# Kernel tuning notes

Measured on AMD Instinct MI355X. Metric: run time of the kernel, lower is better.

Reference implementation:

```python
import jax, jax.numpy as jnp
import numpy as np

B, NN, HL = 64, 64, 50
IN_DIM, POS_DIM, ATT_DIM = 384, 64, 256
NEWS_DIM = IN_DIM + POS_DIM  # 448


def setup_inputs() -> dict:
    key = jax.random.key(0)
    ks = jax.random.split(key, 8)
    pos_emb = jax.random.uniform(ks[3], (100, POS_DIM), jnp.float32, -0.1, 0.1)
    pos_emb = pos_emb.at[0].set(0.0)  # initialize() zeros row 0
    return {
        "log_vec": jax.random.normal(ks[0], (B, HL, IN_DIM), jnp.float32),
        "log_mask": jax.random.randint(ks[1], (B, HL), 0, 2, jnp.int32),
        "news_vec": jax.random.normal(ks[2], (B, NN, IN_DIM), jnp.float32),
        "pos_emb": pos_emb,
        "W1": jax.random.normal(ks[4], (ATT_DIM, 2 * NEWS_DIM), jnp.float32) * 0.02,
        "b1": jnp.zeros((ATT_DIM,), jnp.float32),
        "W2": jax.random.normal(ks[5], (1, ATT_DIM), jnp.float32) * 0.02,
        "b2": jnp.zeros((1,), jnp.float32),
    }


def reference(log_vec, log_mask, news_vec, pos_emb, W1, b1, W2, b2):
    b, nn_ = news_vec.shape[:2]
    hl = log_mask.shape[1]
    # append position embeddings (row 0 for candidates, rows 1..hl for history)
    nf = jnp.concatenate(
        [news_vec, jnp.broadcast_to(pos_emb[0], (b, nn_, POS_DIM))], axis=-1)   # (B,NN,ND)
    lf = jnp.concatenate(
        [log_vec, jnp.broadcast_to(pos_emb[1:hl + 1], (b, hl, POS_DIM))], axis=-1)  # (B,HL,ND)
    # affine1(cat[news, log]) == news @ Wn^T + log @ Wl^T + b1 (avoids concat)
    Wn, Wl = W1[:, :NEWS_DIM], W1[:, NEWS_DIM:]
    pn = jnp.einsum('bnd,ad->bna', nf, Wn)   # (B,NN,A)
    pl = jnp.einsum('bhd,ad->bha', lf, Wl)   # (B,HL,A)
    h = jnp.tanh(pn[:, :, None, :] + pl[:, None, :, :] + b1)  # (B,NN,HL,A)
    logits = jnp.einsum('bnha,a->bnh', h, W2[0]) + b2[0]      # (B,NN,HL)
    logits = jnp.where(log_mask[:, None, :] == 0, jnp.float32(-1e9), logits)
    attn = jax.nn.softmax(logits, axis=2)
    user_log_vecs = jnp.einsum('bnh,bhd->bnd', attn, lf)      # (B,NN,ND)
    return user_log_vecs, nf
```

## Files before the change

### kernel.cpp

```cpp
#include <hip/hip_runtime.h>
#include <math.h>

typedef unsigned short u16;
typedef unsigned int   u32;

#define B_       64
#define NN_      64
#define HL_      50
#define IN_DIM   384
#define POS_DIM  64
#define ATT_DIM  256
#define NEWS_DIM 448

typedef __attribute__((ext_vector_type(8))) short short8;
typedef __attribute__((ext_vector_type(4))) float f32x4;

#if __has_builtin(__builtin_amdgcn_exp2f)
#define EXP2F(x) __builtin_amdgcn_exp2f(x)
#else
#define EXP2F(x) exp2f(x)
#endif
#if __has_builtin(__builtin_amdgcn_rcpf)
#define RCPF(x) __builtin_amdgcn_rcpf(x)
#else
#define RCPF(x) (1.0f/(x))
#endif

__device__ __forceinline__ u16 f2bf(float f) {
    union { float f; u32 i; } v; v.f = f;
    u32 r = v.i + 0x7fffu + ((v.i >> 16) & 1u);
    return (u16)(r >> 16);
}
__device__ __forceinline__ uint2 pack4(float4 v) {
    return make_uint2((u32)f2bf(v.x) | ((u32)f2bf(v.y) << 16),
                      (u32)f2bf(v.z) | ((u32)f2bf(v.w) << 16));
}
__device__ __forceinline__ float fast_tanh(float x) {
    float e = EXP2F(x * 2.88539008f);
    return 1.0f - 2.0f * RCPF(1.0f + e);
}

#define C_W   57344u
#define C_NV  393216u
#define C_LG  307200u
#define C_PS  51200u
#define C_NZ  65536u
#define C_LTZ 28672u
#define C_TOT (C_W + C_NV + C_LG + C_PS + C_NZ + C_LTZ)

__global__ __launch_bounds__(256) void prep_k(
    const float* __restrict__ W1, const float* __restrict__ newsv,
    const float* __restrict__ logv, const float* __restrict__ pos,
    u16* __restrict__ Wbf, u16* __restrict__ nv_bf, u16* __restrict__ lf_bf,
    u16* __restrict__ lfT_bf, float* __restrict__ nf)
{
    u32 i = blockIdx.x * 256u + threadIdx.x;
    if (i < C_W) {
        float4 v = *(const float4*)(W1 + (size_t)i * 4u);
        *(uint2*)(Wbf + (size_t)i * 4u) = pack4(v);
        return;
    }
    i -= C_W;
    if (i < C_NV) {
        float4 v = *(const float4*)(newsv + (size_t)i * 4u);
        *(uint2*)(nv_bf + (size_t)i * 4u) = pack4(v);
        u32 e = i * 4u, r = e / IN_DIM, d = e - r * IN_DIM;
        *(float4*)(nf + (size_t)r * NEWS_DIM + d) = v;
        return;
    }
    i -= C_NV;
    if (i < C_LG) {
        float4 v = *(const float4*)(logv + (size_t)i * 4u);
        u32 e = i * 4u, r = e / IN_DIM, d = e - r * IN_DIM;
        *(uint2*)(lf_bf + (size_t)r * NEWS_DIM + d) = pack4(v);
        u32 b = r / HL_, h = r - b * HL_;
        u16* t = lfT_bf + ((size_t)b * NEWS_DIM + d) * 64u + h;
        t[0]   = f2bf(v.x); t[64]  = f2bf(v.y);
        t[128] = f2bf(v.z); t[192] = f2bf(v.w);
        return;
    }
    i -= C_LG;
    if (i < C_PS) {
        u32 e = i * 4u, r = e / POS_DIM, d = e - r * POS_DIM;
        u32 b = r / HL_, h = r - b * HL_;
        float4 v = *(const float4*)(pos + (size_t)(1u + h) * POS_DIM + d);
        *(uint2*)(lf_bf + (size_t)r * NEWS_DIM + IN_DIM + d) = pack4(v);
        u16* t = lfT_bf + ((size_t)b * NEWS_DIM + IN_DIM + d) * 64u + h;
        t[0]   = f2bf(v.x); t[64]  = f2bf(v.y);
        t[128] = f2bf(v.z); t[192] = f2bf(v.w);
        return;
    }
    i -= C_PS;
    if (i < C_NZ) {
        u32 e = i * 4u, r = e / POS_DIM, d = e - r * POS_DIM;
        *(float4*)(nf + (size_t)r * NEWS_DIM + IN_DIM + d) = make_float4(0.f, 0.f, 0.f, 0.f);
        return;
    }
    i -= C_NZ;
    if (i < C_LTZ) {
        u32* t = (u32*)lfT_bf + (size_t)i * 32u + 25u;
#pragma unroll
        for (int j = 0; j < 7; j++) t[j] = 0u;
    }
}

__global__ __launch_bounds__(64) void gemm_k(
    const u16* __restrict__ nv_bf, const u16* __restrict__ lf_bf,
    const u16* __restrict__ Wbf, const float* __restrict__ b1,
    float* __restrict__ pn, float* __restrict__ plT)
{
    int bid = blockIdx.x;
    int lane = threadIdx.x;
    int m = lane & 15, q = lane >> 4;
    bool is_pn = bid < 256;
    int r0, c0, lda, koff, klen;
    const u16* A;
    if (is_pn) { r0 = (bid & 63) * 64;       c0 = (bid >> 6) * 64; A = nv_bf; lda = IN_DIM;   koff = 0;        klen = IN_DIM; }
    else { int b2 = bid - 256; r0 = (b2 % 50) * 64; c0 = (b2 / 50) * 64; A = lf_bf; lda = NEWS_DIM; koff = NEWS_DIM; klen = NEWS_DIM; }

    f32x4 acc[4][4];
#pragma unroll
    for (int a = 0; a < 4; a++)
#pragma unroll
        for (int b = 0; b < 4; b++) acc[a][b] = (f32x4){0.f, 0.f, 0.f, 0.f};

    const u16* Ap = A + (size_t)(r0 + m) * lda + q * 8;
    const u16* Wp = Wbf + (size_t)(c0 + m) * (2 * NEWS_DIM) + koff + q * 8;

    for (int k = 0; k < klen; k += 32) {
        short8 af[4], wf[4];
#pragma unroll
        for (int rt = 0; rt < 4; rt++) af[rt] = *(const short8*)(Ap + rt * 16 * lda + k);
#pragma unroll
        for (int ct = 0; ct < 4; ct++) wf[ct] = *(const short8*)(Wp + ct * 16 * (2 * NEWS_DIM) + k);
#pragma unroll
        for (int rt = 0; rt < 4; rt++)
#pragma unroll
            for (int ct = 0; ct < 4; ct++)
                acc[rt][ct] = __builtin_amdgcn_mfma_f32_16x16x32_bf16(
                    af[rt], wf[ct], acc[rt][ct], 0, 0, 0);
    }
#pragma unroll
    for (int rt = 0; rt < 4; rt++)
#pragma unroll
        for (int ct = 0; ct < 4; ct++)
#pragma unroll
            for (int i = 0; i < 4; i++) {
                int gr = r0 + rt * 16 + q * 4 + i;
                int gc = c0 + ct * 16 + m;
                float v = acc[rt][ct][i];
                if (is_pn) {
                    pn[(size_t)gr * ATT_DIM + gc] = v + b1[gc];
                } else {
                    int bb = gr / HL_, hh = gr - bb * HL_;
                    plT[(size_t)(bb * ATT_DIM + gc) * HL_ + hh] = v;
                }
            }
}

__global__ __launch_bounds__(256) void attn_k(
    const float* __restrict__ pn, const float* __restrict__ plT,
    const float* __restrict__ w2, const int* __restrict__ lmask,
    u16* __restrict__ attn_bf)
{
    int lane = threadIdx.x & 63;
    int w = (int)(threadIdx.x >> 6);
    int g = blockIdx.x * 4 + w;
    int b = g >> 5;
    int n0 = (g & 31) * 2;
    int hl = (lane < HL_) ? lane : (HL_ - 1);
    const float* pr0 = pn + ((size_t)b * NN_ + n0) * ATT_DIM;
    const float* pr1 = pr0 + ATT_DIM;
    const float* pl = plT + (size_t)b * ATT_DIM * HL_ + hl;

    float a00 = 0.f, a01 = 0.f, a10 = 0.f, a11 = 0.f;
#pragma unroll 2
    for (int a = 0; a < ATT_DIM; a += 4) {
        float4 w4 = *(const float4*)(w2 + a);
        float4 p0 = *(const float4*)(pr0 + a);
        float4 p1 = *(const float4*)(pr1 + a);
        float l0 = pl[(a + 0) * HL_];
        float l1 = pl[(a + 1) * HL_];
        float l2 = pl[(a + 2) * HL_];
        float l3 = pl[(a + 3) * HL_];
        a00 = __builtin_fmaf(fast_tanh(p0.x + l0), w4.x, a00);
        a10 = __builtin_fmaf(fast_tanh(p1.x + l0), w4.x, a10);
        a01 = __builtin_fmaf(fast_tanh(p0.y + l1), w4.y, a01);
        a11 = __builtin_fmaf(fast_tanh(p1.y + l1), w4.y, a11);
        a00 = __builtin_fmaf(fast_tanh(p0.z + l2), w4.z, a00);
        a10 = __builtin_fmaf(fast_tanh(p1.z + l2), w4.z, a10);
        a01 = __builtin_fmaf(fast_tanh(p0.w + l3), w4.w, a01);
        a11 = __builtin_fmaf(fast_tanh(p1.w + l3), w4.w, a11);
    }
    float acc0 = a00 + a01, acc1 = a10 + a11;
    int mv = (lane < HL_) ? lmask[b * HL_ + lane] : 0;
    float lg0 = mv ? acc0 : -1e9f;
    float lg1 = mv ? acc1 : -1e9f;
    float mx0 = lg0, mx1 = lg1;
#pragma unroll
    for (int o = 32; o > 0; o >>= 1) {
        mx0 = fmaxf(mx0, __shfl_xor(mx0, o));
        mx1 = fmaxf(mx1, __shfl_xor(mx1, o));
    }
    float e0 = EXP2F((lg0 - mx0) * 1.44269504f);
    float e1 = EXP2F((lg1 - mx1) * 1.44269504f);
    float s0 = e0, s1 = e1;
#pragma unroll
    for (int o = 32; o > 0; o >>= 1) {
        s0 += __shfl_xor(s0, o);
        s1 += __shfl_xor(s1, o);
    }
    u16* ab = attn_bf + (size_t)b * (NN_ * 64) + (size_t)n0 * 64 + lane;
    ab[0]  = f2bf(e0 * RCPF(s0));
    ab[64] = f2bf(e1 * RCPF(s1));
}

__global__ __launch_bounds__(256) void out_k(
    const u16* __restrict__ attn_bf, const u16* __restrict__ lfT_bf,
    float* __restrict__ out)
{
    int bid = blockIdx.x;
    int b = bid >> 2, quad = bid & 3;
    int w = (int)(threadIdx.x >> 6);
    int lane = threadIdx.x & 63;
    int m = lane & 15, q = lane >> 4;
    int n0 = w * 16;

    const u16* Ap = attn_bf + (size_t)b * (NN_ * 64) + (size_t)(n0 + m) * 64 + q * 8;
    short8 a0 = *(const short8*)(Ap);
    short8 a1 = *(const short8*)(Ap + 32);
    const u16* Bb = lfT_bf + (size_t)b * NEWS_DIM * 64;

#pragma unroll
    for (int dt = 0; dt < 7; dt++) {
        int d0 = quad * 112 + dt * 16;
        const u16* Bp = Bb + (size_t)(d0 + m) * 64 + q * 8;
        short8 b0 = *(const short8*)(Bp);
        short8 b1 = *(const short8*)(Bp + 32);
        f32x4 c = (f32x4){0.f, 0.f, 0.f, 0.f};
        c = __builtin_amdgcn_mfma_f32_16x16x32_bf16(a0, b0, c, 0, 0, 0);
        c = __builtin_amdgcn_mfma_f32_16x16x32_bf16(a1, b1, c, 0, 0, 0);
#pragma unroll
        for (int i = 0; i < 4; i++)
            out[((size_t)b * NN_ + n0 + q * 4 + i) * NEWS_DIM + d0 + m] = c[i];
    }
}

extern "C" void kernel_launch(void* const* d_in, const int* in_sizes, int n_in,
                              void* d_out, int out_size, void* d_ws, size_t ws_size,
                              hipStream_t stream) {
    const float* logv  = (const float*)d_in[0];
    const int*   lmask = (const int*)d_in[1];
    const float* newsv = (const float*)d_in[2];
    const float* pos   = (const float*)d_in[3];
    const float* W1    = (const float*)d_in[4];
    const float* b1    = (const float*)d_in[5];
    const float* w2    = (const float*)d_in[6];

    float* out = (float*)d_out;
    float* nf  = out + (size_t)B_ * NN_ * NEWS_DIM;

    char* ws = (char*)d_ws;
    u16*   lf_bf   = (u16*)(ws + 0);
    u16*   Wbf     = (u16*)(ws + 2867200);
    u16*   nv_bf   = (u16*)(ws + 3325952);
    float* pn      = (float*)(ws + 6471680);
    float* plT     = (float*)(ws + 10665984);
    u16*   lfT_bf  = (u16*)(ws + 13942784);
    u16*   attn_bf = (u16*)(ws + 17612800);

    prep_k<<<C_TOT / 256, 256, 0, stream>>>(W1, newsv, logv, pos,
                                            Wbf, nv_bf, lf_bf, lfT_bf, nf);
    gemm_k<<<456, 64, 0, stream>>>(nv_bf, lf_bf, Wbf, b1, pn, plT);
    attn_k<<<512, 256, 0, stream>>>(pn, plT, w2, lmask, attn_bf);
    out_k <<<256, 256, 0, stream>>>(attn_bf, lfT_bf, out);
}
```

Measured before the change: 137.4 us.

## Fuse attention softmax with output weighted sum and drop transposed log buffer

```diff
diff --git a/kernel.cpp b/kernel.cpp
--- a/kernel.cpp
+++ b/kernel.cpp
@@ -31,6 +31,9 @@
     u32 r = v.i + 0x7fffu + ((v.i >> 16) & 1u);
     return (u16)(r >> 16);
 }
+__device__ __forceinline__ float bf2f(u16 u) {
+    union { u32 i; float f; } v; v.i = ((u32)u) << 16; return v.f;
+}
 __device__ __forceinline__ uint2 pack4(float4 v) {
     return make_uint2((u32)f2bf(v.x) | ((u32)f2bf(v.y) << 16),
                       (u32)f2bf(v.z) | ((u32)f2bf(v.w) << 16));
@@ -45,14 +48,13 @@
 #define C_LG  307200u
 #define C_PS  51200u
 #define C_NZ  65536u
-#define C_LTZ 28672u
-#define C_TOT (C_W + C_NV + C_LG + C_PS + C_NZ + C_LTZ)
+#define C_TOT (C_W + C_NV + C_LG + C_PS + C_NZ)
 
 __global__ __launch_bounds__(256) void prep_k(
     const float* __restrict__ W1, const float* __restrict__ newsv,
     const float* __restrict__ logv, const float* __restrict__ pos,
     u16* __restrict__ Wbf, u16* __restrict__ nv_bf, u16* __restrict__ lf_bf,
-    u16* __restrict__ lfT_bf, float* __restrict__ nf)
+    float* __restrict__ nf)
 {
     u32 i = blockIdx.x * 256u + threadIdx.x;
     if (i < C_W) {
@@ -73,34 +75,20 @@
         float4 v = *(const float4*)(logv + (size_t)i * 4u);
         u32 e = i * 4u, r = e / IN_DIM, d = e - r * IN_DIM;
         *(uint2*)(lf_bf + (size_t)r * NEWS_DIM + d) = pack4(v);
-        u32 b = r / HL_, h = r - b * HL_;
-        u16* t = lfT_bf + ((size_t)b * NEWS_DIM + d) * 64u + h;
-        t[0]   = f2bf(v.x); t[64]  = f2bf(v.y);
-        t[128] = f2bf(v.z); t[192] = f2bf(v.w);
         return;
     }
     i -= C_LG;
     if (i < C_PS) {
         u32 e = i * 4u, r = e / POS_DIM, d = e - r * POS_DIM;
-        u32 b = r / HL_, h = r - b * HL_;
+        u32 h = r % HL_;
         float4 v = *(const float4*)(pos + (size_t)(1u + h) * POS_DIM + d);
         *(uint2*)(lf_bf + (size_t)r * NEWS_DIM + IN_DIM + d) = pack4(v);
-        u16* t = lfT_bf + ((size_t)b * NEWS_DIM + IN_DIM + d) * 64u + h;
-        t[0]   = f2bf(v.x); t[64]  = f2bf(v.y);
-        t[128] = f2bf(v.z); t[192] = f2bf(v.w);
         return;
     }
     i -= C_PS;
     if (i < C_NZ) {
         u32 e = i * 4u, r = e / POS_DIM, d = e - r * POS_DIM;
         *(float4*)(nf + (size_t)r * NEWS_DIM + IN_DIM + d) = make_float4(0.f, 0.f, 0.f, 0.f);
-        return;
-    }
-    i -= C_NZ;
-    if (i < C_LTZ) {
-        u32* t = (u32*)lfT_bf + (size_t)i * 32u + 25u;
-#pragma unroll
-        for (int j = 0; j < 7; j++) t[j] = 0u;
     }
 }
 
@@ -158,14 +146,15 @@
             }
 }
 
-__global__ __launch_bounds__(256) void attn_k(
+__global__ __launch_bounds__(256) void attn_out_k(
     const float* __restrict__ pn, const float* __restrict__ plT,
     const float* __restrict__ w2, const int* __restrict__ lmask,
-    u16* __restrict__ attn_bf)
+    const u16* __restrict__ lf_bf, float* __restrict__ out)
 {
+    __shared__ float at_s[4][2][64];
     int lane = threadIdx.x & 63;
-    int w = (int)(threadIdx.x >> 6);
-    int g = blockIdx.x * 4 + w;
+    int wid = (int)(threadIdx.x >> 6);
+    int g = blockIdx.x * 4 + wid;
     int b = g >> 5;
     int n0 = (g & 31) * 2;
     int hl = (lane < HL_) ? lane : (HL_ - 1);
@@ -210,39 +199,29 @@
         s0 += __shfl_xor(s0, o);
         s1 += __shfl_xor(s1, o);
     }
-    u16* ab = attn_bf + (size_t)b * (NN_ * 64) + (size_t)n0 * 64 + lane;
-    ab[0]  = f2bf(e0 * RCPF(s0));
-    ab[64] = f2bf(e1 * RCPF(s1));
-}
-
-__global__ __launch_bounds__(256) void out_k(
-    const u16* __restrict__ attn_bf, const u16* __restrict__ lfT_bf,
-    float* __restrict__ out)
-{
-    int bid = blockIdx.x;
-    int b = bid >> 2, quad = bid & 3;
-    int w = (int)(threadIdx.x >> 6);
-    int lane = threadIdx.x & 63;
-    int m = lane & 15, q = lane >> 4;
-    int n0 = w * 16;
-
-    const u16* Ap = attn_bf + (size_t)b * (NN_ * 64) + (size_t)(n0 + m) * 64 + q * 8;
-    short8 a0 = *(const short8*)(Ap);
-    short8 a1 = *(const short8*)(Ap + 32);
-    const u16* Bb = lfT_bf + (size_t)b * NEWS_DIM * 64;
-
-#pragma unroll
-    for (int dt = 0; dt < 7; dt++) {
-        int d0 = quad * 112 + dt * 16;
-        const u16* Bp = Bb + (size_t)(d0 + m) * 64 + q * 8;
-        short8 b0 = *(const short8*)(Bp);
-        short8 b1 = *(const short8*)(Bp + 32);
-        f32x4 c = (f32x4){0.f, 0.f, 0.f, 0.f};
-        c = __builtin_amdgcn_mfma_f32_16x16x32_bf16(a0, b0, c, 0, 0, 0);
-        c = __builtin_amdgcn_mfma_f32_16x16x32_bf16(a1, b1, c, 0, 0, 0);
-#pragma unroll
-        for (int i = 0; i < 4; i++)
-            out[((size_t)b * NN_ + n0 + q * 4 + i) * NEWS_DIM + d0 + m] = c[i];
+    at_s[wid][0][lane] = e0 * RCPF(s0);
+    at_s[wid][1][lane] = e1 * RCPF(s1);
+
+    const u16* lfb = lf_bf + (size_t)b * HL_ * NEWS_DIM + lane;
+    float acc[2][7];
+#pragma unroll
+    for (int j = 0; j < 7; j++) { acc[0][j] = 0.f; acc[1][j] = 0.f; }
+    for (int h = 0; h < HL_; h++) {
+        float v0 = at_s[wid][0][h];
+        float v1 = at_s[wid][1][h];
+        const u16* row = lfb + (size_t)h * NEWS_DIM;
+#pragma unroll
+        for (int j = 0; j < 7; j++) {
+            float lv = bf2f(row[64 * j]);
+            acc[0][j] = fmaf(v0, lv, acc[0][j]);
+            acc[1][j] = fmaf(v1, lv, acc[1][j]);
+        }
+    }
+    float* o0 = out + ((size_t)b * NN_ + n0) * NEWS_DIM + lane;
+#pragma unroll
+    for (int j = 0; j < 7; j++) {
+        o0[64 * j] = acc[0][j];
+        o0[NEWS_DIM + 64 * j] = acc[1][j];
     }
 }
 
@@ -261,17 +240,14 @@
     float* nf  = out + (size_t)B_ * NN_ * NEWS_DIM;
 
     char* ws = (char*)d_ws;
-    u16*   lf_bf   = (u16*)(ws + 0);
-    u16*   Wbf     = (u16*)(ws + 2867200);
-    u16*   nv_bf   = (u16*)(ws + 3325952);
-    float* pn      = (float*)(ws + 6471680);
-    float* plT     = (float*)(ws + 10665984);
-    u16*   lfT_bf  = (u16*)(ws + 13942784);
-    u16*   attn_bf = (u16*)(ws + 17612800);
-
-    prep_k<<<C_TOT / 256, 256, 0, stream>>>(W1, newsv, logv, pos,
-                                            Wbf, nv_bf, lf_bf, lfT_bf, nf);
-    gemm_k<<<456, 64, 0, stream>>>(nv_bf, lf_bf, Wbf, b1, pn, plT);
-    attn_k<<<512, 256, 0, stream>>>(pn, plT, w2, lmask, attn_bf);
-    out_k <<<256, 256, 0, stream>>>(attn_bf, lfT_bf, out);
-}
+    u16*   lf_bf = (u16*)(ws + 0);
+    u16*   Wbf   = (u16*)(ws + 2867200);
+    u16*   nv_bf = (u16*)(ws + 3325952);
+    float* pn    = (float*)(ws + 6471680);
+    float* plT   = (float*)(ws + 10665984);
+
+    prep_k    <<<C_TOT / 256, 256, 0, stream>>>(W1, newsv, logv, pos,
+                                                Wbf, nv_bf, lf_bf, nf);
+    gemm_k    <<<456, 64, 0, stream>>>(nv_bf, lf_bf, Wbf, b1, pn, plT);
+    attn_out_k<<<512, 256, 0, stream>>>(pn, plT, w2, lmask, lf_bf, out);
+}
```

New measurement: 134.5 us. -2.1%, faster.
